# Kernel optimization log

Measured on AMD Instinct MI355X. Metric: run time of the kernel, lower is better.

The kernel has to match this reference:

```python
import jax, jax.numpy as jnp
import numpy as np

E = 64      # ENTITY_EMBED_DIM
NH = 4      # ATTN_NUM_HEADS
HD = E // NH
H = 128     # RNN_HIDDEN_SIZE
LN_EPS = 1e-5

def _leaky(x):
    return jnp.where(x >= 0, x, 0.01 * x)

def setup_inputs() -> dict:
    key = jax.random.key(0)
    ks = jax.random.split(key, 20)
    def n(k, shape, s=0.1):
        return (jax.random.normal(k, shape, jnp.float32) * s)
    B, S = 128, 1024
    return {
        'obs': jax.random.normal(ks[0], (B, S, 12), jnp.float32),
        'hidden_state': jnp.zeros((1, B, H), jnp.float32),
        # missile encoder: Linear(3,32) -> LeakyReLU -> Linear(32,64)
        'me_w1': n(ks[1], (32, 3)), 'me_b1': jnp.zeros((32,), jnp.float32),
        'me_w2': n(ks[2], (64, 32)), 'me_b2': jnp.zeros((64,), jnp.float32),
        # aircraft encoder: Linear(6,32) -> LeakyReLU -> Linear(32,64)
        'ae_w1': n(ks[3], (32, 6)), 'ae_b1': jnp.zeros((32,), jnp.float32),
        'ae_w2': n(ks[4], (64, 32)), 'ae_b2': jnp.zeros((64,), jnp.float32),
        # MultiheadAttention packed in_proj (q,k,v) + out_proj
        'in_proj_w': n(ks[5], (3 * E, E)), 'in_proj_b': jnp.zeros((3 * E,), jnp.float32),
        'out_proj_w': n(ks[6], (E, E)), 'out_proj_b': jnp.zeros((E,), jnp.float32),
        # LayerNorm
        'ln_g': jnp.ones((E,), jnp.float32), 'ln_b': jnp.zeros((E,), jnp.float32),
        # GRU (r,z,n gate order, torch convention)
        'gru_w_ih': n(ks[7], (3 * H, E)), 'gru_w_hh': n(ks[8], (3 * H, H)),
        'gru_b_ih': jnp.zeros((3 * H,), jnp.float32), 'gru_b_hh': jnp.zeros((3 * H,), jnp.float32),
        # post-GRU MLP: Linear(128,128)+LeakyReLU x2
        'mlp_w0': n(ks[9], (128, 128)), 'mlp_b0': jnp.zeros((128,), jnp.float32),
        'mlp_w1': n(ks[10], (128, 128)), 'mlp_b1': jnp.zeros((128,), jnp.float32),
        # value head
        'out_w': n(ks[11], (1, 128)), 'out_b': jnp.zeros((1,), jnp.float32),
    }

def reference(obs, hidden_state, me_w1, me_b1, me_w2, me_b2, ae_w1, ae_b1, ae_w2, ae_b2,
              in_proj_w, in_proj_b, out_proj_w, out_proj_b, ln_g, ln_b,
              gru_w_ih, gru_w_hh, gru_b_ih, gru_b_hh,
              mlp_w0, mlp_b0, mlp_w1, mlp_b1, out_w, out_b):
    B, S, _ = obs.shape
    m1 = obs[..., 0:3]
    m2 = obs[..., 3:6]
    ac = obs[..., 6:12]

    def enc(x, w1, b1, w2, b2):
        return _leaky(x @ w1.T + b1) @ w2.T + b2

    m1e = enc(m1, me_w1, me_b1, me_w2, me_b2)   # [B,S,E]
    m2e = enc(m2, me_w1, me_b1, me_w2, me_b2)   # [B,S,E]
    ace = enc(ac, ae_w1, ae_b1, ae_w2, ae_b2)   # [B,S,E]

    # Cross-attention: 1 query (aircraft), 2 keys/values (missiles) per (b,s)
    wq, wk, wv = in_proj_w[:E], in_proj_w[E:2 * E], in_proj_w[2 * E:]
    bq, bk, bv = in_proj_b[:E], in_proj_b[E:2 * E], in_proj_b[2 * E:]
    q = ace @ wq.T + bq                          # [B,S,E]
    kv_in = jnp.stack([m1e, m2e], axis=2)        # [B,S,2,E]
    k = kv_in @ wk.T + bk                        # [B,S,2,E]
    v = kv_in @ wv.T + bv
    qh = q.reshape(B, S, NH, HD)
    kh = k.reshape(B, S, 2, NH, HD)
    vh = v.reshape(B, S, 2, NH, HD)
    scale = 1.0 / np.sqrt(HD)
    scores = jnp.einsum('bshd,bsnhd->bshn', qh, kh) * scale  # [B,S,NH,2]
    attn = jax.nn.softmax(scores, axis=-1)
    ctx = jnp.einsum('bshn,bsnhd->bshd', attn, vh).reshape(B, S, E)
    attn_out = ctx @ out_proj_w.T + out_proj_b

    # residual + LayerNorm
    x = attn_out + ace
    mu = jnp.mean(x, axis=-1, keepdims=True)
    var = jnp.mean((x - mu) ** 2, axis=-1, keepdims=True)
    xn = (x - mu) * jax.lax.rsqrt(var + LN_EPS) * ln_g + ln_b  # [B,S,E]

    # GRU over S (torch gate order r,z,n)
    xp = xn @ gru_w_ih.T + gru_b_ih  # [B,S,3H]

    def step(h, xt):
        hp = h @ gru_w_hh.T + gru_b_hh
        xr, xz, xg = jnp.split(xt, 3, axis=-1)
        hr, hz, hg = jnp.split(hp, 3, axis=-1)
        r = jax.nn.sigmoid(xr + hr)
        z = jax.nn.sigmoid(xz + hz)
        g = jnp.tanh(xg + r * hg)
        h_new = (1.0 - z) * g + z * h
        return h_new, h_new

    h_last, outs = jax.lax.scan(step, hidden_state[0], jnp.swapaxes(xp, 0, 1))
    gru_out = jnp.swapaxes(outs, 0, 1)  # [B,S,H]

    f = _leaky(gru_out @ mlp_w0.T + mlp_b0)
    f = _leaky(f @ mlp_w1.T + mlp_b1)
    value = f @ out_w.T + out_b  # [B,S,1]
    return value, h_last[None]
```

## Files before the change

kernel.cpp:

```cpp
#include <hip/hip_runtime.h>
#include <hip/hip_bf16.h>

#define BB 128
#define SS 1024
#define HH 128
#define G3 384
#define NT (BB * SS)

typedef __hip_bfloat16 bf16;
typedef unsigned int uint;
typedef unsigned short ushort;
typedef _Float16 f16;
typedef f16 f16x2 __attribute__((ext_vector_type(2)));
typedef f16 f16x8 __attribute__((ext_vector_type(8)));
typedef float f32x4 __attribute__((ext_vector_type(4)));

__device__ __forceinline__ float leaky(float x) { return x >= 0.f ? x : 0.01f * x; }
__device__ __forceinline__ f16x2 u2h(uint u) { return __builtin_bit_cast(f16x2, u); }
__device__ __forceinline__ uint packh2(float a, float b) {
  f16x2 h; h.x = (f16)a; h.y = (f16)b;
  return __builtin_bit_cast(uint, h);
}
__device__ __forceinline__ uint h1(float a) {
  return (uint)__builtin_bit_cast(ushort, (f16)a);
}
__device__ __forceinline__ uint bf_rne(float f) {
  uint u = __float_as_uint(f);
  return (u + 0x7FFFu + ((u >> 16) & 1u)) >> 16;
}
__device__ __forceinline__ float shflx(float v, int m) { return __shfl_xor(v, m, 64); }
__device__ __forceinline__ uint dpp_xor1_u(uint v) {
  int i = __builtin_amdgcn_update_dpp(0, (int)v, 0xB1, 0xF, 0xF, true);
  return (uint)i;
}
#define WSYNC() asm volatile("s_waitcnt lgkmcnt(0)" ::: "memory")

template <int NP>
__device__ __forceinline__ void ldrow(const float* __restrict__ p, f16x2* w) {
#pragma unroll
  for (int i = 0; i < NP; ++i) {
    f16x2 h; h.x = (f16)p[2 * i]; h.y = (f16)p[2 * i + 1];
    w[i] = h;
  }
}
__device__ __forceinline__ f16x8 ldw8(const float* __restrict__ p) {
  f16x8 v;
#pragma unroll
  for (int j = 0; j < 8; ++j) v[j] = (f16)p[j];
  return v;
}
template <int NP>
__device__ __forceinline__ float dot2l(const uint* __restrict__ x,
                                       const f16x2* __restrict__ w, float acc) {
#pragma unroll
  for (int i = 0; i < NP / 4; ++i) {
    uint4 uu = ((const uint4*)x)[i];
    acc = __builtin_amdgcn_fdot2(u2h(uu.x), w[4 * i + 0], acc, false);
    acc = __builtin_amdgcn_fdot2(u2h(uu.y), w[4 * i + 1], acc, false);
    acc = __builtin_amdgcn_fdot2(u2h(uu.z), w[4 * i + 2], acc, false);
    acc = __builtin_amdgcn_fdot2(u2h(uu.w), w[4 * i + 3], acc, false);
  }
  return acc;
}
__device__ __forceinline__ float d4(uint4 x, uint4 w, float acc) {
  acc = __builtin_amdgcn_fdot2(u2h(x.x), u2h(w.x), acc, false);
  acc = __builtin_amdgcn_fdot2(u2h(x.y), u2h(w.y), acc, false);
  acc = __builtin_amdgcn_fdot2(u2h(x.z), u2h(w.z), acc, false);
  acc = __builtin_amdgcn_fdot2(u2h(x.w), u2h(w.w), acc, false);
  return acc;
}

__global__ __launch_bounds__(256, 4) void pre_a(
    const float* __restrict__ obs, const float* __restrict__ me_w1,
    const float* __restrict__ me_b1, const float* __restrict__ me_w2,
    const float* __restrict__ me_b2, const float* __restrict__ ae_w1,
    const float* __restrict__ ae_b1, const float* __restrict__ ae_w2,
    const float* __restrict__ ae_b2, const float* __restrict__ ipw,
    const float* __restrict__ ipb, const float* __restrict__ opw,
    const float* __restrict__ opb, const float* __restrict__ lng,
    const float* __restrict__ lnb, uint* __restrict__ xnh) {
  __shared__ float ss[352];
  __shared__ __align__(16) uint4 w4[8 * 256];
  __shared__ __align__(16) uint ex[4][176];

  const int tid = threadIdx.x;
  const int wid = tid >> 6, l = tid & 63;
  if (tid < 96) ss[tid] = me_w1[tid];
  if (tid < 32) ss[96 + tid] = me_b1[tid];
  if (tid < 192) ss[128 + tid] = ae_w1[tid];
  if (tid < 32) ss[320 + tid] = ae_b1[tid];

  for (int idx = tid; idx < 2048; idx += 256) {
    const int r = idx & 255, c = idx >> 8;
    const float* src =
        (r < 192 ? ipw + (size_t)r * 64 : opw + (size_t)(r - 192) * 64) + c * 8;
    uint4 u;
    u.x = packh2(src[0], src[1]);
    u.y = packh2(src[2], src[3]);
    u.z = packh2(src[4], src[5]);
    u.w = packh2(src[6], src[7]);
    w4[(c << 8) + r] = u;
  }

  f16x2 wme2[16], wae2[16];
  ldrow<16>(me_w2 + l * 32, wme2);
  ldrow<16>(ae_w2 + l * 32, wae2);
  const float bme2 = me_b2[l], bae2 = ae_b2[l];
  const float bq = ipb[l], bk = ipb[64 + l], bv = ipb[128 + l], bop = opb[l];
  const float gl = lng[l], bl = lnb[l];
  __syncthreads();

  uint* um = ex[wid];
  uint* ua = um + 32;
  uint* e1 = um + 48;
  uint* e2 = um + 80;
  uint* ea = um + 112;
  uint* ec = um + 144;

  for (int base = blockIdx.x * 4; base < NT; base += 4096) {
    const size_t token = base + wid;
    const float4* ob4 = (const float4*)(obs + token * 12);
    float4 o0 = ob4[0], o1 = ob4[1], o2 = ob4[2];

    const int row = l & 31;
    const bool m2h = l >= 32;
    float i0 = m2h ? o0.w : o0.x, i1 = m2h ? o1.x : o0.y, i2 = m2h ? o1.y : o0.z;
    float t1 = ss[96 + row] + i0 * ss[row * 3] + i1 * ss[row * 3 + 1] + i2 * ss[row * 3 + 2];
    t1 = leaky(t1);
    float ta = ss[320 + row] + o1.z * ss[128 + row * 6] + o1.w * ss[128 + row * 6 + 1] +
               o2.x * ss[128 + row * 6 + 2] + o2.y * ss[128 + row * 6 + 3] +
               o2.z * ss[128 + row * 6 + 4] + o2.w * ss[128 + row * 6 + 5];
    ta = leaky(ta);
    float t1p = shflx(t1, 1), tap = shflx(ta, 1);
    if (!(l & 1)) {
      um[l >> 1] = packh2(t1, t1p);
      if (l < 32) ua[l >> 1] = packh2(ta, tap);
    }
    WSYNC();

    float m1e = dot2l<16>(um, wme2, bme2);
    float m2e = dot2l<16>(um + 16, wme2, bme2);
    float ace = dot2l<16>(ua, wae2, bae2);
    float m1p = shflx(m1e, 1), m2p = shflx(m2e, 1), acp = shflx(ace, 1);
    if (!(l & 1)) {
      e1[l >> 1] = packh2(m1e, m1p);
      e2[l >> 1] = packh2(m2e, m2p);
      ea[l >> 1] = packh2(ace, acp);
    }
    WSYNC();

    float q = bq, k1 = bk, k2 = bk, v1 = bv, v2 = bv;
    {
      const uint4* xe1 = (const uint4*)e1;
      const uint4* xe2 = (const uint4*)e2;
      const uint4* xea = (const uint4*)ea;
#pragma unroll
      for (int c = 0; c < 8; ++c) {
        uint4 x1 = xe1[c], x2 = xe2[c], xa = xea[c];
        uint4 uq = w4[(c << 8) + l];
        uint4 uk = w4[(c << 8) + 64 + l];
        uint4 uv = w4[(c << 8) + 128 + l];
        q = d4(xa, uq, q);
        k1 = d4(x1, uk, k1);
        k2 = d4(x2, uk, k2);
        v1 = d4(x1, uv, v1);
        v2 = d4(x2, uv, v2);
      }
    }

    float p1 = q * k1, p2 = q * k2;
    p1 += shflx(p1, 1); p2 += shflx(p2, 1);
    p1 += shflx(p1, 2); p2 += shflx(p2, 2);
    p1 += shflx(p1, 4); p2 += shflx(p2, 4);
    p1 += shflx(p1, 8); p2 += shflx(p2, 8);
    float s1 = p1 * 0.25f, s2 = p2 * 0.25f;
    float mx = fmaxf(s1, s2);
    float ev1 = __expf(s1 - mx), ev2 = __expf(s2 - mx);
    float a1 = ev1 / (ev1 + ev2);
    float ctx = a1 * v1 + (1.f - a1) * v2;
    float cxp = shflx(ctx, 1);
    if (!(l & 1)) ec[l >> 1] = packh2(ctx, cxp);
    WSYNC();

    float ao = bop;
    {
      const uint4* xec = (const uint4*)ec;
#pragma unroll
      for (int c = 0; c < 8; ++c) {
        ao = d4(xec[c], w4[(c << 8) + 192 + l], ao);
      }
    }
    float x = ao + ace;
    float s = x, s2s = x * x;
#pragma unroll
    for (int off = 32; off; off >>= 1) {
      s += shflx(s, off);
      s2s += shflx(s2s, off);
    }
    float mu = s * (1.f / 64.f);
    float var = s2s * (1.f / 64.f) - mu * mu;
    float rs = rsqrtf(var + 1e-5f);
    float xn = (x - mu) * rs * gl + bl;
    float xnp = shflx(xn, 1);
    if (!(l & 1)) xnh[token * 32 + (l >> 1)] = packh2(xn, xnp);
  }
}

__global__ __launch_bounds__(256) void pre_b(const uint* __restrict__ xnh,
                                             const float* __restrict__ wih,
                                             const float* __restrict__ bih,
                                             uint* __restrict__ xp32) {
  const int tid = threadIdx.x;
  const int l = tid & 63, wv = tid >> 6;
  const int n16 = l & 15, q = l >> 4;

  f16x8 Bf[6][2];
  float bias_l[6];
#pragma unroll
  for (int i = 0; i < 6; ++i) {
    const int n = (wv * 6 + i) * 16 + n16;
    const float* wrow = wih + (size_t)n * 64;
    Bf[i][0] = ldw8(wrow + q * 8);
    Bf[i][1] = ldw8(wrow + 32 + q * 8);
    bias_l[i] = bih[n];
  }

  for (int tile = blockIdx.x; tile < NT / 16; tile += gridDim.x) {
    const uint4* arow = (const uint4*)(xnh + (size_t)(tile * 16 + n16) * 32);
    f16x8 A0 = __builtin_bit_cast(f16x8, arow[q]);
    f16x8 A1 = __builtin_bit_cast(f16x8, arow[4 + q]);
#pragma unroll
    for (int i = 0; i < 6; ++i) {
      const int nt = wv * 6 + i;
      f32x4 acc = {0.f, 0.f, 0.f, 0.f};
      acc = __builtin_amdgcn_mfma_f32_16x16x32_f16(A0, Bf[i][0], acc, 0, 0, 0);
      acc = __builtin_amdgcn_mfma_f32_16x16x32_f16(A1, Bf[i][1], acc, 0, 0, 0);
#pragma unroll
      for (int r = 0; r < 4; ++r) {
        uint bv = bf_rne(acc[r] + bias_l[i]);
        uint pv = dpp_xor1_u(bv);
        if (!(l & 1))
          xp32[(size_t)(tile * 16 + q * 4 + r) * 192 + nt * 8 + (n16 >> 1)] =
              bv | (pv << 16);
      }
    }
  }
}

__global__ __launch_bounds__(320, 1) void gru_kernel(
    const bf16* __restrict__ xp, const float* __restrict__ hs,
    const float* __restrict__ whh, const float* __restrict__ bhh,
    ushort* __restrict__ gouth, float* __restrict__ hlast) {
  __shared__ __align__(16) ushort hbuf[2][HH];
  __shared__ __align__(16) uint ring[8 * 192];
  const int tid = threadIdx.x;
  const int b = blockIdx.x;
  const bool comp = tid < 256;
  const int lane = tid & 63;
  const int w = tid >> 6;
  const int n16 = lane & 15, q = lane >> 4;
  const int pid = tid - 256;

  f16x8 Bf[6][4];
  float bias_r = 0.f, bias_z = 0.f, bias_g = 0.f, hp = 0.f;
  int idx = 0;
  const uint* xr32 = (const uint*)(xp + (size_t)b * SS * G3);
  uint a0 = 0, a1 = 0, a2 = 0, c0 = 0, c1 = 0, c2 = 0;
  if (comp) {
    const int tn[6] = {2 * w, 2 * w + 1, 8 + 2 * w, 9 + 2 * w, 16 + 2 * w, 17 + 2 * w};
#pragma unroll
    for (int i = 0; i < 6; ++i) {
      const float* wrow = whh + (size_t)(tn[i] * 16 + n16) * HH;
#pragma unroll
      for (int kt = 0; kt < 4; ++kt) Bf[i][kt] = ldw8(wrow + kt * 32 + q * 8);
    }
    idx = 32 * w + n16 + ((q >> 1) ? 16 : 0);
    bias_r = bhh[idx];
    bias_z = bhh[HH + idx];
    bias_g = bhh[2 * HH + idx];
    hp = hs[b * HH + idx];
    if (tid < HH) hbuf[0][tid] = (ushort)h1(hs[b * HH + tid]);
  } else {
    for (int s = 0; s < 4; ++s) {
      const uint* p = xr32 + s * 192 + pid * 3;
      uint v0 = p[0], v1 = p[1], v2 = p[2];
      uint* qq = ring + s * 192 + pid * 3;
      qq[0] = v0; qq[1] = v1; qq[2] = v2;
    }
    const uint* pa = xr32 + 4 * 192 + pid * 3;
    a0 = pa[0]; a1 = pa[1]; a2 = pa[2];
    const uint* pb = xr32 + 5 * 192 + pid * 3;
    c0 = pb[0]; c1 = pb[1]; c2 = pb[2];
  }
  __syncthreads();

  const ushort* ring_us = (const ushort*)ring;
  ushort* grow = gouth + (size_t)b * SS * HH;
  const bool pub = comp && !(q & 1);
  const int sel = q >> 1;

#define CSTEP(TT, RD, WRI)                                                     \
  {                                                                            \
    const int slot = (TT) & 7;                                                 \
    const uint4* hb = (const uint4*)hbuf[RD];                                  \
    f16x8 A0 = __builtin_bit_cast(f16x8, hb[q]);                               \
    f16x8 A1 = __builtin_bit_cast(f16x8, hb[4 + q]);                           \
    f16x8 A2 = __builtin_bit_cast(f16x8, hb[8 + q]);                           \
    f16x8 A3 = __builtin_bit_cast(f16x8, hb[12 + q]);                          \
    f32x4 ac0 = {0.f, 0.f, 0.f, 0.f}, ac1 = ac0, ac2 = ac0, ac3 = ac0,         \
          ac4 = ac0, ac5 = ac0;                                                \
    ac0 = __builtin_amdgcn_mfma_f32_16x16x32_f16(A0, Bf[0][0], ac0, 0, 0, 0);  \
    ac1 = __builtin_amdgcn_mfma_f32_16x16x32_f16(A0, Bf[1][0], ac1, 0, 0, 0);  \
    ac2 = __builtin_amdgcn_mfma_f32_16x16x32_f16(A0, Bf[2][0], ac2, 0, 0, 0);  \
    ac3 = __builtin_amdgcn_mfma_f32_16x16x32_f16(A0, Bf[3][0], ac3, 0, 0, 0);  \
    ac4 = __builtin_amdgcn_mfma_f32_16x16x32_f16(A0, Bf[4][0], ac4, 0, 0, 0);  \
    ac5 = __builtin_amdgcn_mfma_f32_16x16x32_f16(A0, Bf[5][0], ac5, 0, 0, 0);  \
    ac0 = __builtin_amdgcn_mfma_f32_16x16x32_f16(A1, Bf[0][1], ac0, 0, 0, 0);  \
    ac1 = __builtin_amdgcn_mfma_f32_16x16x32_f16(A1, Bf[1][1], ac1, 0, 0, 0);  \
    ac2 = __builtin_amdgcn_mfma_f32_16x16x32_f16(A1, Bf[2][1], ac2, 0, 0, 0);  \
    ac3 = __builtin_amdgcn_mfma_f32_16x16x32_f16(A1, Bf[3][1], ac3, 0, 0, 0);  \
    ac4 = __builtin_amdgcn_mfma_f32_16x16x32_f16(A1, Bf[4][1], ac4, 0, 0, 0);  \
    ac5 = __builtin_amdgcn_mfma_f32_16x16x32_f16(A1, Bf[5][1], ac5, 0, 0, 0);  \
    ac0 = __builtin_amdgcn_mfma_f32_16x16x32_f16(A2, Bf[0][2], ac0, 0, 0, 0);  \
    ac1 = __builtin_amdgcn_mfma_f32_16x16x32_f16(A2, Bf[1][2], ac1, 0, 0, 0);  \
    ac2 = __builtin_amdgcn_mfma_f32_16x16x32_f16(A2, Bf[2][2], ac2, 0, 0, 0);  \
    ac3 = __builtin_amdgcn_mfma_f32_16x16x32_f16(A2, Bf[3][2], ac3, 0, 0, 0);  \
    ac4 = __builtin_amdgcn_mfma_f32_16x16x32_f16(A2, Bf[4][2], ac4, 0, 0, 0);  \
    ac5 = __builtin_amdgcn_mfma_f32_16x16x32_f16(A2, Bf[5][2], ac5, 0, 0, 0);  \
    ac0 = __builtin_amdgcn_mfma_f32_16x16x32_f16(A3, Bf[0][3], ac0, 0, 0, 0);  \
    ac1 = __builtin_amdgcn_mfma_f32_16x16x32_f16(A3, Bf[1][3], ac1, 0, 0, 0);  \
    ac2 = __builtin_amdgcn_mfma_f32_16x16x32_f16(A3, Bf[2][3], ac2, 0, 0, 0);  \
    ac3 = __builtin_amdgcn_mfma_f32_16x16x32_f16(A3, Bf[3][3], ac3, 0, 0, 0);  \
    ac4 = __builtin_amdgcn_mfma_f32_16x16x32_f16(A3, Bf[4][3], ac4, 0, 0, 0);  \
    ac5 = __builtin_amdgcn_mfma_f32_16x16x32_f16(A3, Bf[5][3], ac5, 0, 0, 0);  \
    float Pr = (sel ? ac1[0] : ac0[0]) + bias_r;                               \
    float Pz = (sel ? ac3[0] : ac2[0]) + bias_z;                               \
    float Pg = (sel ? ac5[0] : ac4[0]) + bias_g;                               \
    uint bxr = ring_us[slot * 384 + idx];                                      \
    uint bxz = ring_us[slot * 384 + 128 + idx];                                \
    uint bxg = ring_us[slot * 384 + 256 + idx];                                \
    float r = 1.f / (1.f + __expf(-(__uint_as_float(bxr << 16) + Pr)));        \
    float z = 1.f / (1.f + __expf(-(__uint_as_float(bxz << 16) + Pz)));        \
    float gp = __uint_as_float(bxg << 16) + r * Pg;                            \
    float e = __expf(-2.f * fabsf(gp));                                        \
    float th = copysignf((1.f - e) / (1.f + e), gp);                           \
    float hn = (1.f - z) * th + z * hp;                                        \
    hp = hn;                                                                   \
    if (pub) {                                                                 \
      ushort hb16 = (ushort)h1(hn);                                            \
      hbuf[WRI][idx] = hb16;                                                   \
      grow[(size_t)(TT)*HH + idx] = hb16;                                      \
    }                                                                          \
  }

#define PSTEP(TT, R0, R1, R2)                                                  \
  {                                                                            \
    const int wrow = (TT) + 4;                                                 \
    if (wrow < SS) {                                                           \
      uint* qq = ring + (wrow & 7) * 192 + pid * 3;                            \
      qq[0] = R0; qq[1] = R1; qq[2] = R2;                                      \
      const int lrow = (TT) + 6;                                               \
      if (lrow < SS) {                                                         \
        const uint* p = xr32 + lrow * 192 + pid * 3;                           \
        R0 = p[0]; R1 = p[1]; R2 = p[2];                                       \
      }                                                                        \
    }                                                                          \
  }

  for (int t = 0; t < SS; t += 2) {
    if (comp) {
      CSTEP(t, 0, 1);
    } else {
      PSTEP(t, a0, a1, a2);
    }
    asm volatile("s_waitcnt lgkmcnt(0)\n\ts_barrier" ::: "memory");
    if (comp) {
      CSTEP(t + 1, 1, 0);
    } else {
      PSTEP(t + 1, c0, c1, c2);
    }
    asm volatile("s_waitcnt lgkmcnt(0)\n\ts_barrier" ::: "memory");
  }
#undef CSTEP
#undef PSTEP
  if (pub) hlast[b * HH + idx] = hp;
}

__global__ __launch_bounds__(256) void mlp0(const uint* __restrict__ gh,
                                            const float* __restrict__ w0,
                                            const float* __restrict__ b0,
                                            uint* __restrict__ f0h32) {
  const int tid = threadIdx.x;
  const int l = tid & 63, wv = tid >> 6;
  const int n16 = l & 15, q = l >> 4;

  f16x8 Bf[2][4];
  float bias_l[2];
#pragma unroll
  for (int i = 0; i < 2; ++i) {
    const int n = (wv * 2 + i) * 16 + n16;
    const float* wrow = w0 + (size_t)n * 128;
#pragma unroll
    for (int f = 0; f < 4; ++f) Bf[i][f] = ldw8(wrow + f * 32 + q * 8);
    bias_l[i] = b0[n];
  }

  for (int tile = blockIdx.x; tile < NT / 16; tile += gridDim.x) {
    const uint4* arow = (const uint4*)(gh + (size_t)(tile * 16 + n16) * 64);
    f16x8 A[4];
#pragma unroll
    for (int f = 0; f < 4; ++f) A[f] = __builtin_bit_cast(f16x8, arow[f * 4 + q]);
#pragma unroll
    for (int i = 0; i < 2; ++i) {
      const int nt = wv * 2 + i;
      f32x4 acc = {0.f, 0.f, 0.f, 0.f};
#pragma unroll
      for (int f = 0; f < 4; ++f)
        acc = __builtin_amdgcn_mfma_f32_16x16x32_f16(A[f], Bf[i][f], acc, 0, 0, 0);
#pragma unroll
      for (int r = 0; r < 4; ++r) {
        uint hv = h1(leaky(acc[r] + bias_l[i]));
        uint pv = dpp_xor1_u(hv);
        if (!(l & 1))
          f0h32[(size_t)(tile * 16 + q * 4 + r) * 64 + nt * 8 + (n16 >> 1)] =
              hv | (pv << 16);
      }
    }
  }
}

__global__ __launch_bounds__(256) void mlp1(const uint* __restrict__ f0h,
                                            const float* __restrict__ w1,
                                            const float* __restrict__ b1,
                                            const float* __restrict__ ow,
                                            const float* __restrict__ obp,
                                            float* __restrict__ value) {
  const int tid = threadIdx.x;
  const int l = tid & 63, wv = tid >> 6;
  const int n16 = l & 15, q = l >> 4;

  f16x8 Bf[8][4];
  float bias_l[8], ow_l[8];
#pragma unroll
  for (int nt = 0; nt < 8; ++nt) {
    const int n = nt * 16 + n16;
    const float* wrow = w1 + (size_t)n * 128;
#pragma unroll
    for (int f = 0; f < 4; ++f) Bf[nt][f] = ldw8(wrow + f * 32 + q * 8);
    bias_l[nt] = b1[n];
    ow_l[nt] = ow[n];
  }
  const float obias = obp[0];

  for (int tile = blockIdx.x * 4 + wv; tile < NT / 16; tile += gridDim.x * 4) {
    const uint4* arow = (const uint4*)(f0h + (size_t)(tile * 16 + n16) * 64);
    f16x8 A[4];
#pragma unroll
    for (int f = 0; f < 4; ++f) A[f] = __builtin_bit_cast(f16x8, arow[f * 4 + q]);
    float s0 = 0.f, s1 = 0.f, s2 = 0.f, s3 = 0.f;
#pragma unroll
    for (int nt = 0; nt < 8; ++nt) {
      f32x4 acc = {0.f, 0.f, 0.f, 0.f};
#pragma unroll
      for (int f = 0; f < 4; ++f)
        acc = __builtin_amdgcn_mfma_f32_16x16x32_f16(A[f], Bf[nt][f], acc, 0, 0, 0);
      s0 += leaky(acc[0] + bias_l[nt]) * ow_l[nt];
      s1 += leaky(acc[1] + bias_l[nt]) * ow_l[nt];
      s2 += leaky(acc[2] + bias_l[nt]) * ow_l[nt];
      s3 += leaky(acc[3] + bias_l[nt]) * ow_l[nt];
    }
#pragma unroll
    for (int mask = 1; mask < 16; mask <<= 1) {
      s0 += shflx(s0, mask);
      s1 += shflx(s1, mask);
      s2 += shflx(s2, mask);
      s3 += shflx(s3, mask);
    }
    if (n16 == 0) {
      value[tile * 16 + q * 4 + 0] = s0 + obias;
      value[tile * 16 + q * 4 + 1] = s1 + obias;
      value[tile * 16 + q * 4 + 2] = s2 + obias;
      value[tile * 16 + q * 4 + 3] = s3 + obias;
    }
  }
}

__global__ void fill_sentinel(float* o, int n) {
  for (int i = blockIdx.x * blockDim.x + threadIdx.x; i < n; i += gridDim.x * blockDim.x)
    o[i] = 999.0f;
}

extern "C" void kernel_launch(void* const* d_in, const int* in_sizes, int n_in,
                              void* d_out, int out_size, void* d_ws, size_t ws_size,
                              hipStream_t stream) {
  const float* obs = (const float*)d_in[0];
  const float* hs = (const float*)d_in[1];
  const float* me_w1 = (const float*)d_in[2];
  const float* me_b1 = (const float*)d_in[3];
  const float* me_w2 = (const float*)d_in[4];
  const float* me_b2 = (const float*)d_in[5];
  const float* ae_w1 = (const float*)d_in[6];
  const float* ae_b1 = (const float*)d_in[7];
  const float* ae_w2 = (const float*)d_in[8];
  const float* ae_b2 = (const float*)d_in[9];
  const float* ipw = (const float*)d_in[10];
  const float* ipb = (const float*)d_in[11];
  const float* opw = (const float*)d_in[12];
  const float* opb = (const float*)d_in[13];
  const float* lng = (const float*)d_in[14];
  const float* lnb = (const float*)d_in[15];
  const float* wih = (const float*)d_in[16];
  const float* whh = (const float*)d_in[17];
  const float* bih = (const float*)d_in[18];
  const float* bhh = (const float*)d_in[19];
  const float* w0 = (const float*)d_in[20];
  const float* b0 = (const float*)d_in[21];
  const float* w1 = (const float*)d_in[22];
  const float* b1 = (const float*)d_in[23];
  const float* ow = (const float*)d_in[24];
  const float* ob = (const float*)d_in[25];

  const size_t regA_bytes = (size_t)NT * G3 * sizeof(bf16);
  const size_t regB_bytes = (size_t)NT * 64 * sizeof(uint);
  const size_t need = regA_bytes + regB_bytes;
  float* out = (float*)d_out;
  if (ws_size < need) {
    fill_sentinel<<<288, 256, 0, stream>>>(out, out_size);
    return;
  }

  char* ws = (char*)d_ws;
  bf16* xp = (bf16*)ws;
  uint* f0h = (uint*)ws;
  uint* xnh = (uint*)(ws + regA_bytes);
  ushort* gouth = (ushort*)(ws + regA_bytes);

  pre_a<<<1024, 256, 0, stream>>>(obs, me_w1, me_b1, me_w2, me_b2, ae_w1, ae_b1,
                                  ae_w2, ae_b2, ipw, ipb, opw, opb, lng, lnb, xnh);
  pre_b<<<1024, 256, 0, stream>>>(xnh, wih, bih, (uint*)xp);
  gru_kernel<<<BB, 320, 0, stream>>>(xp, hs, whh, bhh, gouth, out + NT);
  mlp0<<<1024, 256, 0, stream>>>((const uint*)gouth, w0, b0, f0h);
  mlp1<<<1024, 256, 0, stream>>>(f0h, w1, b1, ow, ob, out);
}
```

Before: 787.3 us.

## Fuse post-GRU MLP and value head into the GRU recurrence kernel

Stages 16 GRU outputs in shared memory and, every 16 steps, runs both MLP layers and the value head inside the GRU kernel using preloaded weight fragments. This removes the mlp0/mlp1 launches and the round trip of GRU outputs and intermediate activations through global memory. It adds MFMA work and two extra barriers to the serial recurrence loop, which can lengthen the critical path. The tanh is also simplified to a single exp-based form.

```diff
diff --git a/kernel.cpp b/kernel.cpp
--- a/kernel.cpp
+++ b/kernel.cpp
@@ -250,9 +250,15 @@
 __global__ __launch_bounds__(320, 1) void gru_kernel(
     const bf16* __restrict__ xp, const float* __restrict__ hs,
     const float* __restrict__ whh, const float* __restrict__ bhh,
-    ushort* __restrict__ gouth, float* __restrict__ hlast) {
+    const float* __restrict__ w0, const float* __restrict__ b0,
+    const float* __restrict__ w1, const float* __restrict__ b1,
+    const float* __restrict__ ow, const float* __restrict__ obp,
+    float* __restrict__ value, float* __restrict__ hlast) {
   __shared__ __align__(16) ushort hbuf[2][HH];
   __shared__ __align__(16) uint ring[8 * 192];
+  __shared__ __align__(16) ushort hstage[16][HH];
+  __shared__ __align__(16) ushort f0stage[16][HH];
+  __shared__ float vpart[64];
   const int tid = threadIdx.x;
   const int b = blockIdx.x;
   const bool comp = tid < 256;
@@ -262,8 +268,11 @@
   const int pid = tid - 256;
 
   f16x8 Bf[6][4];
+  f16x8 Bm0[2][4], Bm1[2][4];
   float bias_r = 0.f, bias_z = 0.f, bias_g = 0.f, hp = 0.f;
+  float mb0[2] = {0.f, 0.f}, mb1[2] = {0.f, 0.f}, owl[2] = {0.f, 0.f};
   int idx = 0;
+  const float obias = obp[0];
   const uint* xr32 = (const uint*)(xp + (size_t)b * SS * G3);
   uint a0 = 0, a1 = 0, a2 = 0, c0 = 0, c1 = 0, c2 = 0;
   if (comp) {
@@ -273,6 +282,18 @@
       const float* wrow = whh + (size_t)(tn[i] * 16 + n16) * HH;
 #pragma unroll
       for (int kt = 0; kt < 4; ++kt) Bf[i][kt] = ldw8(wrow + kt * 32 + q * 8);
+    }
+#pragma unroll
+    for (int i = 0; i < 2; ++i) {
+      const int n = (2 * w + i) * 16 + n16;
+#pragma unroll
+      for (int f = 0; f < 4; ++f) {
+        Bm0[i][f] = ldw8(w0 + (size_t)n * HH + f * 32 + q * 8);
+        Bm1[i][f] = ldw8(w1 + (size_t)n * HH + f * 32 + q * 8);
+      }
+      mb0[i] = b0[n];
+      mb1[i] = b1[n];
+      owl[i] = ow[n];
     }
     idx = 32 * w + n16 + ((q >> 1) ? 16 : 0);
     bias_r = bhh[idx];
@@ -295,7 +316,6 @@
   __syncthreads();
 
   const ushort* ring_us = (const ushort*)ring;
-  ushort* grow = gouth + (size_t)b * SS * HH;
   const bool pub = comp && !(q & 1);
   const int sel = q >> 1;
 
@@ -342,14 +362,13 @@
     float r = 1.f / (1.f + __expf(-(__uint_as_float(bxr << 16) + Pr)));        \
     float z = 1.f / (1.f + __expf(-(__uint_as_float(bxz << 16) + Pz)));        \
     float gp = __uint_as_float(bxg << 16) + r * Pg;                            \
-    float e = __expf(-2.f * fabsf(gp));                                        \
-    float th = copysignf((1.f - e) / (1.f + e), gp);                           \
+    float th = 2.f / (1.f + __expf(-2.f * gp)) - 1.f;                          \
     float hn = (1.f - z) * th + z * hp;                                        \
     hp = hn;                                                                   \
     if (pub) {                                                                 \
       ushort hb16 = (ushort)h1(hn);                                            \
       hbuf[WRI][idx] = hb16;                                                   \
-      grow[(size_t)(TT)*HH + idx] = hb16;                                      \
+      hstage[(TT) & 15][idx] = hb16;                                           \
     }                                                                          \
   }
 
@@ -367,122 +386,82 @@
     }                                                                          \
   }
 
-  for (int t = 0; t < SS; t += 2) {
+  for (int t0 = 0; t0 < SS; t0 += 16) {
+    for (int u = 0; u < 16; u += 2) {
+      const int t = t0 + u;
+      if (comp) {
+        CSTEP(t, 0, 1);
+      } else {
+        PSTEP(t, a0, a1, a2);
+      }
+      asm volatile("s_waitcnt lgkmcnt(0)\n\ts_barrier" ::: "memory");
+      if (comp) {
+        CSTEP(t + 1, 1, 0);
+      } else {
+        PSTEP(t + 1, c0, c1, c2);
+      }
+      asm volatile("s_waitcnt lgkmcnt(0)\n\ts_barrier" ::: "memory");
+    }
     if (comp) {
-      CSTEP(t, 0, 1);
-    } else {
-      PSTEP(t, a0, a1, a2);
+      const uint4* hs4 = (const uint4*)hstage;
+      f16x8 A[4];
+#pragma unroll
+      for (int f = 0; f < 4; ++f)
+        A[f] = __builtin_bit_cast(f16x8, hs4[n16 * 16 + f * 4 + q]);
+#pragma unroll
+      for (int i = 0; i < 2; ++i) {
+        f32x4 acc = {0.f, 0.f, 0.f, 0.f};
+#pragma unroll
+        for (int f = 0; f < 4; ++f)
+          acc = __builtin_amdgcn_mfma_f32_16x16x32_f16(A[f], Bm0[i][f], acc, 0, 0, 0);
+#pragma unroll
+        for (int r = 0; r < 4; ++r)
+          f0stage[q * 4 + r][(2 * w + i) * 16 + n16] =
+              (ushort)h1(leaky(acc[r] + mb0[i]));
+      }
     }
     asm volatile("s_waitcnt lgkmcnt(0)\n\ts_barrier" ::: "memory");
     if (comp) {
-      CSTEP(t + 1, 1, 0);
-    } else {
-      PSTEP(t + 1, c0, c1, c2);
+      const uint4* fs4 = (const uint4*)f0stage;
+      f16x8 A[4];
+#pragma unroll
+      for (int f = 0; f < 4; ++f)
+        A[f] = __builtin_bit_cast(f16x8, fs4[n16 * 16 + f * 4 + q]);
+      float s0 = 0.f, s1 = 0.f, s2 = 0.f, s3 = 0.f;
+#pragma unroll
+      for (int i = 0; i < 2; ++i) {
+        f32x4 acc = {0.f, 0.f, 0.f, 0.f};
+#pragma unroll
+        for (int f = 0; f < 4; ++f)
+          acc = __builtin_amdgcn_mfma_f32_16x16x32_f16(A[f], Bm1[i][f], acc, 0, 0, 0);
+        s0 += leaky(acc[0] + mb1[i]) * owl[i];
+        s1 += leaky(acc[1] + mb1[i]) * owl[i];
+        s2 += leaky(acc[2] + mb1[i]) * owl[i];
+        s3 += leaky(acc[3] + mb1[i]) * owl[i];
+      }
+#pragma unroll
+      for (int m = 1; m < 16; m <<= 1) {
+        s0 += shflx(s0, m);
+        s1 += shflx(s1, m);
+        s2 += shflx(s2, m);
+        s3 += shflx(s3, m);
+      }
+      if (n16 == 0) {
+        vpart[w * 16 + q * 4 + 0] = s0;
+        vpart[w * 16 + q * 4 + 1] = s1;
+        vpart[w * 16 + q * 4 + 2] = s2;
+        vpart[w * 16 + q * 4 + 3] = s3;
+      }
     }
     asm volatile("s_waitcnt lgkmcnt(0)\n\ts_barrier" ::: "memory");
+    if (tid < 16) {
+      float v = vpart[tid] + vpart[16 + tid] + vpart[32 + tid] + vpart[48 + tid] + obias;
+      value[(size_t)b * SS + t0 + tid] = v;
+    }
   }
 #undef CSTEP
 #undef PSTEP
   if (pub) hlast[b * HH + idx] = hp;
-}
-
-__global__ __launch_bounds__(256) void mlp0(const uint* __restrict__ gh,
-                                            const float* __restrict__ w0,
-                                            const float* __restrict__ b0,
-                                            uint* __restrict__ f0h32) {
-  const int tid = threadIdx.x;
-  const int l = tid & 63, wv = tid >> 6;
-  const int n16 = l & 15, q = l >> 4;
-
-  f16x8 Bf[2][4];
-  float bias_l[2];
-#pragma unroll
-  for (int i = 0; i < 2; ++i) {
-    const int n = (wv * 2 + i) * 16 + n16;
-    const float* wrow = w0 + (size_t)n * 128;
-#pragma unroll
-    for (int f = 0; f < 4; ++f) Bf[i][f] = ldw8(wrow + f * 32 + q * 8);
-    bias_l[i] = b0[n];
-  }
-
-  for (int tile = blockIdx.x; tile < NT / 16; tile += gridDim.x) {
-    const uint4* arow = (const uint4*)(gh + (size_t)(tile * 16 + n16) * 64);
-    f16x8 A[4];
-#pragma unroll
-    for (int f = 0; f < 4; ++f) A[f] = __builtin_bit_cast(f16x8, arow[f * 4 + q]);
-#pragma unroll
-    for (int i = 0; i < 2; ++i) {
-      const int nt = wv * 2 + i;
-      f32x4 acc = {0.f, 0.f, 0.f, 0.f};
-#pragma unroll
-      for (int f = 0; f < 4; ++f)
-        acc = __builtin_amdgcn_mfma_f32_16x16x32_f16(A[f], Bf[i][f], acc, 0, 0, 0);
-#pragma unroll
-      for (int r = 0; r < 4; ++r) {
-        uint hv = h1(leaky(acc[r] + bias_l[i]));
-        uint pv = dpp_xor1_u(hv);
-        if (!(l & 1))
-          f0h32[(size_t)(tile * 16 + q * 4 + r) * 64 + nt * 8 + (n16 >> 1)] =
-              hv | (pv << 16);
-      }
-    }
-  }
-}
-
-__global__ __launch_bounds__(256) void mlp1(const uint* __restrict__ f0h,
-                                            const float* __restrict__ w1,
-                                            const float* __restrict__ b1,
-                                            const float* __restrict__ ow,
-                                            const float* __restrict__ obp,
-                                            float* __restrict__ value) {
-  const int tid = threadIdx.x;
-  const int l = tid & 63, wv = tid >> 6;
-  const int n16 = l & 15, q = l >> 4;
-
-  f16x8 Bf[8][4];
-  float bias_l[8], ow_l[8];
-#pragma unroll
-  for (int nt = 0; nt < 8; ++nt) {
-    const int n = nt * 16 + n16;
-    const float* wrow = w1 + (size_t)n * 128;
-#pragma unroll
-    for (int f = 0; f < 4; ++f) Bf[nt][f] = ldw8(wrow + f * 32 + q * 8);
-    bias_l[nt] = b1[n];
-    ow_l[nt] = ow[n];
-  }
-  const float obias = obp[0];
-
-  for (int tile = blockIdx.x * 4 + wv; tile < NT / 16; tile += gridDim.x * 4) {
-    const uint4* arow = (const uint4*)(f0h + (size_t)(tile * 16 + n16) * 64);
-    f16x8 A[4];
-#pragma unroll
-    for (int f = 0; f < 4; ++f) A[f] = __builtin_bit_cast(f16x8, arow[f * 4 + q]);
-    float s0 = 0.f, s1 = 0.f, s2 = 0.f, s3 = 0.f;
-#pragma unroll
-    for (int nt = 0; nt < 8; ++nt) {
-      f32x4 acc = {0.f, 0.f, 0.f, 0.f};
-#pragma unroll
-      for (int f = 0; f < 4; ++f)
-        acc = __builtin_amdgcn_mfma_f32_16x16x32_f16(A[f], Bf[nt][f], acc, 0, 0, 0);
-      s0 += leaky(acc[0] + bias_l[nt]) * ow_l[nt];
-      s1 += leaky(acc[1] + bias_l[nt]) * ow_l[nt];
-      s2 += leaky(acc[2] + bias_l[nt]) * ow_l[nt];
-      s3 += leaky(acc[3] + bias_l[nt]) * ow_l[nt];
-    }
-#pragma unroll
-    for (int mask = 1; mask < 16; mask <<= 1) {
-      s0 += shflx(s0, mask);
-      s1 += shflx(s1, mask);
-      s2 += shflx(s2, mask);
-      s3 += shflx(s3, mask);
-    }
-    if (n16 == 0) {
-      value[tile * 16 + q * 4 + 0] = s0 + obias;
-      value[tile * 16 + q * 4 + 1] = s1 + obias;
-      value[tile * 16 + q * 4 + 2] = s2 + obias;
-      value[tile * 16 + q * 4 + 3] = s3 + obias;
-    }
-  }
 }
 
 __global__ void fill_sentinel(float* o, int n) {
@@ -531,14 +510,11 @@
 
   char* ws = (char*)d_ws;
   bf16* xp = (bf16*)ws;
-  uint* f0h = (uint*)ws;
   uint* xnh = (uint*)(ws + regA_bytes);
-  ushort* gouth = (ushort*)(ws + regA_bytes);
 
   pre_a<<<1024, 256, 0, stream>>>(obs, me_w1, me_b1, me_w2, me_b2, ae_w1, ae_b1,
                                   ae_w2, ae_b2, ipw, ipb, opw, opb, lng, lnb, xnh);
   pre_b<<<1024, 256, 0, stream>>>(xnh, wih, bih, (uint*)xp);
-  gru_kernel<<<BB, 320, 0, stream>>>(xp, hs, whh, bhh, gouth, out + NT);
-  mlp0<<<1024, 256, 0, stream>>>((const uint*)gouth, w0, b0, f0h);
-  mlp1<<<1024, 256, 0, stream>>>(f0h, w1, b1, ow, ob, out);
-}
+  gru_kernel<<<BB, 320, 0, stream>>>(xp, hs, whh, bhh, w0, b0, w1, b1, ow, ob,
+                                     out, out + NT);
+}
```

Result: no change. 799.3 us (+1.5%).
